# Performance work log

Measured on AMD Instinct MI355X. Metric: run time of the kernel, lower is better.

## Reference

```python
import jax, jax.numpy as jnp
import numpy as np

H_IN, W_IN = 128, 128  # sensor grid; region=(1,1), stride=(1,1) -> one RF per pixel


def setup_inputs() -> dict:
    key = jax.random.key(0)
    k1, k2, k3, k4, k5, k6 = jax.random.split(key, 6)
    B, N, C, HID = 8, 2048, 16, 128
    s = 1.0 / np.sqrt(HID)
    features = jax.random.normal(k1, (B, N, C), dtype=jnp.float32)
    coords = jax.random.randint(k2, (B, N, 2), 0, 128, dtype=jnp.int32)  # (x, y)
    w_ih = jax.random.normal(k3, (4 * HID, C), dtype=jnp.float32) * s
    w_hh = jax.random.normal(k4, (4 * HID, HID), dtype=jnp.float32) * s
    b_ih = jax.random.normal(k5, (4 * HID,), dtype=jnp.float32) * s
    b_hh = jax.random.normal(k6, (4 * HID,), dtype=jnp.float32) * s
    return {"features": features, "coords": coords, "w_ih": w_ih,
            "w_hh": w_hh, "b_ih": b_ih, "b_hh": b_hh}


def reference(features, coords, w_ih, w_hh, b_ih, b_hh):
    """MatrixLSTM with 1x1 non-overlapping receptive fields.

    Events (time-ordered along axis 1) are routed to their pixel's RF; a shared
    LSTM is run over each RF's event sequence and the last output per RF is
    scattered into a dense [B, hidden, H, W] map (zeros where no events).
    Implemented as one lax.scan over events with per-RF (h, c) state.
    """
    B, N, C = features.shape
    HID = w_hh.shape[1]
    # coord2idx: raster order y * W + x  -> RF id per event, [B, N]
    rf = coords[:, :, 1].astype(jnp.int32) * W_IN + coords[:, :, 0].astype(jnp.int32)
    bidx = jnp.arange(B)
    bias = b_ih + b_hh

    def step(carry, inp):
        h_all, c_all = carry              # [B, num_rf, HID] each
        x_t, rf_t = inp                   # [B, C], [B]
        h_prev = h_all[bidx, rf_t]        # gather per-RF state, [B, HID]
        c_prev = c_all[bidx, rf_t]
        gates = x_t @ w_ih.T + h_prev @ w_hh.T + bias  # [B, 4*HID]
        i, f, g, o = jnp.split(gates, 4, axis=-1)       # torch LSTM gate order
        i = jax.nn.sigmoid(i)
        f = jax.nn.sigmoid(f)
        g = jnp.tanh(g)
        o = jax.nn.sigmoid(o)
        c_new = f * c_prev + i * g
        h_new = o * jnp.tanh(c_new)
        h_all = h_all.at[bidx, rf_t].set(h_new)        # scatter back
        c_all = c_all.at[bidx, rf_t].set(c_new)
        return (h_all, c_all), None

    h0 = jnp.zeros((B, H_IN * W_IN, HID), features.dtype)
    c0 = jnp.zeros_like(h0)
    (h_all, _), _ = jax.lax.scan(step, (h0, c0),
                                 (features.transpose(1, 0, 2), rf.T))
    # final h per RF == LSTM output at each RF's last event; zeros if no events
    return h_all.reshape(B, H_IN, W_IN, HID).transpose(0, 3, 1, 2)
```

## Files before the change

kernel.cpp:

```cpp
#include <hip/hip_runtime.h>
#include <hip/hip_bf16.h>
#include <math.h>

#define B 8
#define N 2048
#define C 16
#define HID 128
#define NRF 16384
#define MAXLEN 8
#define MAXCH 2048

__global__ void k_init(int* __restrict__ cntrf, int* __restrict__ map,
                       int* __restrict__ cnt) {
    int i = blockIdx.x * blockDim.x + threadIdx.x;
    if (i < B * NRF) { cntrf[i] = 0; map[i] = -1; }
    if (i < B) cnt[i] = 0;
}

__global__ void k_prep(const float* __restrict__ w_ih, const float* __restrict__ w_hh,
                       const float* __restrict__ b_ih, const float* __restrict__ b_hh,
                       float* __restrict__ w_ih_T, float* __restrict__ w_hh_T,
                       float* __restrict__ biassum) {
    int idx = blockIdx.x * blockDim.x + threadIdx.x;
    if (idx < C * 512) {
        int c = idx >> 9, j = idx & 511;
        w_ih_T[idx] = w_ih[j * C + c];
    } else if (idx < C * 512 + HID * 512) {
        int t = idx - C * 512;
        int k = t >> 9, j = t & 511;
        w_hh_T[t] = w_hh[j * HID + k];
    } else if (idx < C * 512 + HID * 512 + 512) {
        int j = idx - (C * 512 + HID * 512);
        biassum[j] = b_ih[j] + b_hh[j];
    }
}

__global__ __launch_bounds__(256) void k_build(
    const int* __restrict__ coords, int* __restrict__ cntrf,
    int* __restrict__ map, int* __restrict__ cnt,
    int* __restrict__ chainrf, int* __restrict__ slots) {
    int idx = blockIdx.x * blockDim.x + threadIdx.x;
    int b = idx >> 11;
    int n = idx & (N - 1);
    int x = coords[idx * 2 + 0];
    int y = coords[idx * 2 + 1];
    int rf = y * 128 + x;
    int pos = atomicAdd(&cntrf[b * NRF + rf], 1);
    if (pos < MAXLEN) slots[(b * NRF + rf) * MAXLEN + pos] = n;

    __shared__ int lcnt, lbase;
    if (threadIdx.x == 0) lcnt = 0;
    __syncthreads();
    int r = -1;
    if (pos == 0) r = atomicAdd(&lcnt, 1);
    __syncthreads();
    if (threadIdx.x == 0) lbase = atomicAdd(&cnt[b], lcnt);
    __syncthreads();
    if (pos == 0) {
        int k = lbase + r;
        chainrf[b * MAXCH + k] = rf;
        map[b * NRF + rf] = k;
    }
}

__global__ __launch_bounds__(256) void k_gates(
    const float* __restrict__ features, const float* __restrict__ w_ih_T,
    const float* __restrict__ biassum, float* __restrict__ gates_x) {
    __shared__ float ls_w[C * 512];
    __shared__ float ls_b[512];
    __shared__ float ls_x[64 * C];
    int tid = threadIdx.x;
    for (int i = tid; i < C * 512; i += 256) ls_w[i] = w_ih_T[i];
    if (tid < 256) { ls_b[tid] = biassum[tid]; ls_b[tid + 256] = biassum[tid + 256]; }
    int e0 = blockIdx.x * 64;
    for (int i = tid; i < 64 * C; i += 256) ls_x[i] = features[e0 * C + i];
    __syncthreads();
    float b0 = ls_b[tid], b1 = ls_b[tid + 256];
    for (int e = 0; e < 64; e++) {
        float a0 = b0, a1 = b1;
#pragma unroll
        for (int ci = 0; ci < C; ci++) {
            float xv = ls_x[e * C + ci];
            a0 += ls_w[ci * 512 + tid] * xv;
            a1 += ls_w[ci * 512 + tid + 256] * xv;
        }
        gates_x[(size_t)(e0 + e) * 512 + tid] = a0;
        gates_x[(size_t)(e0 + e) * 512 + tid + 256] = a1;
    }
}

__global__ __launch_bounds__(64) void k_lstm(
    const float* __restrict__ gates_x, const float* __restrict__ w_hh_T,
    const int* __restrict__ cnt, const int* __restrict__ chainrf,
    const int* __restrict__ cntrf, const int* __restrict__ slots,
    float* __restrict__ hfin) {
    int b = blockIdx.x >> 9;
    int j0 = blockIdx.x & 511;
    int lane = threadIdx.x;
    __shared__ float lds_h[HID];
    int nch = cnt[b];
    for (int j = j0; j < nch; j += 512) {
        int rf = chainrf[b * MAXCH + j];
        int len = cntrf[b * NRF + rf];
        if (len > MAXLEN) len = MAXLEN;
        const int* sl = slots + (size_t)(b * NRF + rf) * MAXLEN;
        int ev[MAXLEN];
#pragma unroll
        for (int t = 0; t < MAXLEN; t++) {
            int v = sl[t];
            ev[t] = (t < len) ? v : 0x7fffffff;
        }
#pragma unroll
        for (int a = 0; a < MAXLEN; a++)
#pragma unroll
            for (int q = 0; q < MAXLEN - 1; q++) {
                int u = ev[q], v = ev[q + 1];
                ev[q] = min(u, v);
                ev[q + 1] = max(u, v);
            }
        float c0 = 0.f, c1 = 0.f, h0 = 0.f, h1 = 0.f;
#pragma unroll
        for (int t = 0; t < MAXLEN; t++) {
            if (t >= len) break;
            int n = ev[t];
            const float* gx = gates_x + (size_t)(b * N + n) * 512;
            float acc[8];
#pragma unroll
            for (int r = 0; r < 8; r++) acc[r] = gx[lane + 64 * r];
            if (t > 0) {
                for (int k = 0; k < HID; k += 2) {
                    float hv0 = lds_h[k];
                    float hv1 = lds_h[k + 1];
#pragma unroll
                    for (int r = 0; r < 8; r++)
                        acc[r] += w_hh_T[k * 512 + lane + 64 * r] * hv0;
#pragma unroll
                    for (int r = 0; r < 8; r++)
                        acc[r] += w_hh_T[(k + 1) * 512 + lane + 64 * r] * hv1;
                }
            }
            float i0 = 1.f / (1.f + expf(-acc[0]));
            float i1 = 1.f / (1.f + expf(-acc[1]));
            float f0 = 1.f / (1.f + expf(-acc[2]));
            float f1 = 1.f / (1.f + expf(-acc[3]));
            float g0 = tanhf(acc[4]);
            float g1 = tanhf(acc[5]);
            float o0 = 1.f / (1.f + expf(-acc[6]));
            float o1 = 1.f / (1.f + expf(-acc[7]));
            c0 = f0 * c0 + i0 * g0;
            c1 = f1 * c1 + i1 * g1;
            h0 = o0 * tanhf(c0);
            h1 = o1 * tanhf(c1);
            if (t + 1 < len) {
                __syncthreads();
                lds_h[lane] = h0;
                lds_h[lane + 64] = h1;
                __syncthreads();
            }
        }
        hfin[(size_t)(b * MAXCH + j) * HID + lane] = h0;
        hfin[(size_t)(b * MAXCH + j) * HID + lane + 64] = h1;
    }
}

__global__ __launch_bounds__(256) void k_scatter(
    const float* __restrict__ hfin, const int* __restrict__ map,
    float* __restrict__ out) {
    int b = blockIdx.x >> 7;
    int y = blockIdx.x & 127;
    int t = threadIdx.x;
    int xq = t & 31;
    int hg = t >> 5;
    const int4* mrow = (const int4*)(map + b * NRF + y * 128);
    int4 kk = mrow[xq];
    const float* hb = hfin + (size_t)b * MAXCH * HID;
#pragma unroll
    for (int hh = 0; hh < 16; hh++) {
        int hid = hg * 16 + hh;
        float4 v;
        v.x = (kk.x < 0) ? 0.f : hb[kk.x * HID + hid];
        v.y = (kk.y < 0) ? 0.f : hb[kk.y * HID + hid];
        v.z = (kk.z < 0) ? 0.f : hb[kk.z * HID + hid];
        v.w = (kk.w < 0) ? 0.f : hb[kk.w * HID + hid];
        *(float4*)(out + ((((size_t)b * HID + hid) * 128 + y) * 128) + xq * 4) = v;
    }
}

extern "C" void kernel_launch(void* const* d_in, const int* in_sizes, int n_in,
                              void* d_out, int out_size, void* d_ws, size_t ws_size,
                              hipStream_t stream) {
    const float* features = (const float*)d_in[0];
    const int*   coords   = (const int*)d_in[1];
    const float* w_ih     = (const float*)d_in[2];
    const float* w_hh     = (const float*)d_in[3];
    const float* b_ih     = (const float*)d_in[4];
    const float* b_hh     = (const float*)d_in[5];
    float* out = (float*)d_out;

    char* ws = (char*)d_ws;
    float* w_ih_T  = (float*)(ws + 0);
    float* w_hh_T  = (float*)(ws + 32768);
    float* biassum = (float*)(ws + 294912);
    int*   cntrf   = (int*)(ws + 296960);
    int*   map     = (int*)(ws + 821248);
    int*   cnt     = (int*)(ws + 1345536);
    int*   chainrf = (int*)(ws + 1345600);
    int*   slots   = (int*)(ws + 1411136);
    float* hfin    = (float*)(ws + 5605440);
    float* gates_x = (float*)(ws + 13994048);

    k_init<<<dim3((B * NRF + 255) / 256), dim3(256), 0, stream>>>(cntrf, map, cnt);
    k_prep<<<dim3((C * 512 + HID * 512 + 512 + 255) / 256), dim3(256), 0, stream>>>(
        w_ih, w_hh, b_ih, b_hh, w_ih_T, w_hh_T, biassum);
    k_build<<<dim3(B * N / 256), dim3(256), 0, stream>>>(
        coords, cntrf, map, cnt, chainrf, slots);
    k_gates<<<dim3(B * N / 64), dim3(256), 0, stream>>>(
        features, w_ih_T, biassum, gates_x);
    k_lstm<<<dim3(B * 512), dim3(64), 0, stream>>>(
        gates_x, w_hh_T, cnt, chainrf, cntrf, slots, hfin);
    k_scatter<<<dim3(B * 128), dim3(256), 0, stream>>>(hfin, map, out);
}
```

Baseline: 158.0 us.

## Split LSTM into single-event fast path and compacted multi-event kernel

```diff
diff --git a/kernel.cpp b/kernel.cpp
--- a/kernel.cpp
+++ b/kernel.cpp
@@ -10,72 +10,67 @@
 #define MAXLEN 8
 #define MAXCH 2048
 
-__global__ void k_init(int* __restrict__ cntrf, int* __restrict__ map,
-                       int* __restrict__ cnt) {
+__global__ __launch_bounds__(256) void k_setup(
+    const float* __restrict__ w_ih, const float* __restrict__ w_hh,
+    const float* __restrict__ b_ih, const float* __restrict__ b_hh,
+    float* __restrict__ w_ih_T, float* __restrict__ w_hh_T,
+    float* __restrict__ biassum, int* __restrict__ cntrf,
+    int* __restrict__ map, int* __restrict__ cnt, int* __restrict__ mcnt) {
     int i = blockIdx.x * blockDim.x + threadIdx.x;
-    if (i < B * NRF) { cntrf[i] = 0; map[i] = -1; }
+    cntrf[i] = 0;
+    map[i] = -1;
     if (i < B) cnt[i] = 0;
-}
-
-__global__ void k_prep(const float* __restrict__ w_ih, const float* __restrict__ w_hh,
-                       const float* __restrict__ b_ih, const float* __restrict__ b_hh,
-                       float* __restrict__ w_ih_T, float* __restrict__ w_hh_T,
-                       float* __restrict__ biassum) {
-    int idx = blockIdx.x * blockDim.x + threadIdx.x;
-    if (idx < C * 512) {
-        int c = idx >> 9, j = idx & 511;
-        w_ih_T[idx] = w_ih[j * C + c];
-    } else if (idx < C * 512 + HID * 512) {
-        int t = idx - C * 512;
-        int k = t >> 9, j = t & 511;
-        w_hh_T[t] = w_hh[j * HID + k];
-    } else if (idx < C * 512 + HID * 512 + 512) {
-        int j = idx - (C * 512 + HID * 512);
-        biassum[j] = b_ih[j] + b_hh[j];
-    }
-}
-
-__global__ __launch_bounds__(256) void k_build(
-    const int* __restrict__ coords, int* __restrict__ cntrf,
-    int* __restrict__ map, int* __restrict__ cnt,
-    int* __restrict__ chainrf, int* __restrict__ slots) {
-    int idx = blockIdx.x * blockDim.x + threadIdx.x;
-    int b = idx >> 11;
-    int n = idx & (N - 1);
-    int x = coords[idx * 2 + 0];
-    int y = coords[idx * 2 + 1];
-    int rf = y * 128 + x;
-    int pos = atomicAdd(&cntrf[b * NRF + rf], 1);
-    if (pos < MAXLEN) slots[(b * NRF + rf) * MAXLEN + pos] = n;
-
+    if (i == 0) mcnt[0] = 0;
+    if (i < C * 512) {
+        int c = i >> 9, j = i & 511;
+        w_ih_T[i] = w_ih[j * C + c];
+    }
+    if (i < HID * 512) {
+        int k = i >> 9, j = i & 511;
+        w_hh_T[i] = w_hh[j * HID + k];
+    }
+    if (i < 512) biassum[i] = b_ih[i] + b_hh[i];
+}
+
+__global__ __launch_bounds__(256) void k_buildgates(
+    const int* __restrict__ coords, const float* __restrict__ features,
+    const float* __restrict__ w_ih_T, const float* __restrict__ biassum,
+    int* __restrict__ cntrf, int* __restrict__ map, int* __restrict__ cnt,
+    int* __restrict__ chainrf, int* __restrict__ slots,
+    float* __restrict__ gates_x) {
+    int tid = threadIdx.x;
     __shared__ int lcnt, lbase;
-    if (threadIdx.x == 0) lcnt = 0;
-    __syncthreads();
-    int r = -1;
-    if (pos == 0) r = atomicAdd(&lcnt, 1);
-    __syncthreads();
-    if (threadIdx.x == 0) lbase = atomicAdd(&cnt[b], lcnt);
-    __syncthreads();
-    if (pos == 0) {
-        int k = lbase + r;
-        chainrf[b * MAXCH + k] = rf;
-        map[b * NRF + rf] = k;
-    }
-}
-
-__global__ __launch_bounds__(256) void k_gates(
-    const float* __restrict__ features, const float* __restrict__ w_ih_T,
-    const float* __restrict__ biassum, float* __restrict__ gates_x) {
     __shared__ float ls_w[C * 512];
-    __shared__ float ls_b[512];
     __shared__ float ls_x[64 * C];
-    int tid = threadIdx.x;
+
+    if (blockIdx.x < 64) {
+        int idx = blockIdx.x * 256 + tid;
+        int b = idx >> 11;
+        int n = idx & (N - 1);
+        int x = coords[idx * 2 + 0];
+        int y = coords[idx * 2 + 1];
+        int rf = y * 128 + x;
+        int pos = atomicAdd(&cntrf[b * NRF + rf], 1);
+        if (pos < MAXLEN) slots[(b * NRF + rf) * MAXLEN + pos] = n;
+        if (tid == 0) lcnt = 0;
+        __syncthreads();
+        int r = -1;
+        if (pos == 0) r = atomicAdd(&lcnt, 1);
+        __syncthreads();
+        if (tid == 0) lbase = atomicAdd(&cnt[b], lcnt);
+        __syncthreads();
+        if (pos == 0) {
+            int k = lbase + r;
+            chainrf[b * MAXCH + k] = rf;
+            map[b * NRF + rf] = k;
+        }
+    }
+
     for (int i = tid; i < C * 512; i += 256) ls_w[i] = w_ih_T[i];
-    if (tid < 256) { ls_b[tid] = biassum[tid]; ls_b[tid + 256] = biassum[tid + 256]; }
     int e0 = blockIdx.x * 64;
     for (int i = tid; i < 64 * C; i += 256) ls_x[i] = features[e0 * C + i];
-    __syncthreads();
-    float b0 = ls_b[tid], b1 = ls_b[tid + 256];
+    float b0 = biassum[tid], b1 = biassum[tid + 256];
+    __syncthreads();
     for (int e = 0; e < 64; e++) {
         float a0 = b0, a1 = b1;
 #pragma unroll
@@ -89,21 +84,79 @@
     }
 }
 
-__global__ __launch_bounds__(64) void k_lstm(
+__global__ __launch_bounds__(256) void k_classify(
+    const int* __restrict__ cnt, const int* __restrict__ chainrf,
+    const int* __restrict__ cntrf, int* __restrict__ mcnt,
+    int* __restrict__ mlist_brf, int* __restrict__ mlist_dst) {
+    int tid = threadIdx.x;
+    int idx = blockIdx.x * 256 + tid;
+    int b = idx >> 11, j = idx & (MAXCH - 1);
+    __shared__ int lcnt, lbase;
+    __shared__ int lbrf[256], ldst[256];
+    int len = 0, rf = 0;
+    if (j < cnt[b]) {
+        rf = chainrf[idx];
+        len = cntrf[b * NRF + rf];
+    }
+    if (tid == 0) lcnt = 0;
+    __syncthreads();
+    if (len >= 2) {
+        int r = atomicAdd(&lcnt, 1);
+        lbrf[r] = b * NRF + rf;
+        ldst[r] = idx;
+    }
+    __syncthreads();
+    if (tid == 0) lbase = atomicAdd(mcnt, lcnt);
+    __syncthreads();
+    for (int i = tid; i < lcnt; i += 256) {
+        mlist_brf[lbase + i] = lbrf[i];
+        mlist_dst[lbase + i] = ldst[i];
+    }
+}
+
+__global__ __launch_bounds__(256) void k_single(
+    const float* __restrict__ gates_x, const int* __restrict__ cnt,
+    const int* __restrict__ chainrf, const int* __restrict__ cntrf,
+    const int* __restrict__ slots, float* __restrict__ hfin) {
+    int lane = threadIdx.x & 63;
+    int wid = blockIdx.x * 4 + (threadIdx.x >> 6);
+    for (int ci = wid; ci < B * MAXCH; ci += 8192) {
+        int b = ci >> 11, j = ci & (MAXCH - 1);
+        if (j >= cnt[b]) continue;
+        int rf = chainrf[ci];
+        if (cntrf[b * NRF + rf] != 1) continue;
+        int n = slots[(size_t)(b * NRF + rf) * MAXLEN];
+        const float* gx = gates_x + (size_t)(b * N + n) * 512;
+        float i0 = gx[lane],       i1 = gx[lane + 64];
+        float g0 = gx[lane + 256], g1 = gx[lane + 320];
+        float o0 = gx[lane + 384], o1 = gx[lane + 448];
+        i0 = 1.f / (1.f + expf(-i0));
+        i1 = 1.f / (1.f + expf(-i1));
+        float c0 = i0 * tanhf(g0);
+        float c1 = i1 * tanhf(g1);
+        float h0 = (1.f / (1.f + expf(-o0))) * tanhf(c0);
+        float h1 = (1.f / (1.f + expf(-o1))) * tanhf(c1);
+        hfin[(size_t)ci * HID + lane] = h0;
+        hfin[(size_t)ci * HID + lane + 64] = h1;
+    }
+}
+
+__global__ __launch_bounds__(256) void k_multi(
     const float* __restrict__ gates_x, const float* __restrict__ w_hh_T,
-    const int* __restrict__ cnt, const int* __restrict__ chainrf,
-    const int* __restrict__ cntrf, const int* __restrict__ slots,
-    float* __restrict__ hfin) {
-    int b = blockIdx.x >> 9;
-    int j0 = blockIdx.x & 511;
-    int lane = threadIdx.x;
-    __shared__ float lds_h[HID];
-    int nch = cnt[b];
-    for (int j = j0; j < nch; j += 512) {
-        int rf = chainrf[b * MAXCH + j];
-        int len = cntrf[b * NRF + rf];
+    const int* __restrict__ mcnt, const int* __restrict__ mlist_brf,
+    const int* __restrict__ mlist_dst, const int* __restrict__ cntrf,
+    const int* __restrict__ slots, float* __restrict__ hfin) {
+    __shared__ float g512[512];
+    __shared__ float hbuf[HID];
+    int tid = threadIdx.x;
+    int M = mcnt[0];
+    for (int m = blockIdx.x; m < M; m += gridDim.x) {
+        int brf = mlist_brf[m];
+        int dst = mlist_dst[m];
+        int b = brf >> 14;
+        int len = cntrf[brf];
         if (len > MAXLEN) len = MAXLEN;
-        const int* sl = slots + (size_t)(b * NRF + rf) * MAXLEN;
+        const int* sl = slots + (size_t)brf * MAXLEN;
         int ev[MAXLEN];
 #pragma unroll
         for (int t = 0; t < MAXLEN; t++) {
@@ -118,48 +171,32 @@
                 ev[q] = min(u, v);
                 ev[q + 1] = max(u, v);
             }
-        float c0 = 0.f, c1 = 0.f, h0 = 0.f, h1 = 0.f;
-#pragma unroll
-        for (int t = 0; t < MAXLEN; t++) {
-            if (t >= len) break;
-            int n = ev[t];
-            const float* gx = gates_x + (size_t)(b * N + n) * 512;
-            float acc[8];
-#pragma unroll
-            for (int r = 0; r < 8; r++) acc[r] = gx[lane + 64 * r];
+        float c = 0.f;
+        for (int t = 0; t < len; t++) {
+            const float* gx = gates_x + (size_t)(b * N + ev[t]) * 512;
+            float a0 = gx[tid], a1 = gx[tid + 256];
             if (t > 0) {
-                for (int k = 0; k < HID; k += 2) {
-                    float hv0 = lds_h[k];
-                    float hv1 = lds_h[k + 1];
-#pragma unroll
-                    for (int r = 0; r < 8; r++)
-                        acc[r] += w_hh_T[k * 512 + lane + 64 * r] * hv0;
-#pragma unroll
-                    for (int r = 0; r < 8; r++)
-                        acc[r] += w_hh_T[(k + 1) * 512 + lane + 64 * r] * hv1;
+#pragma unroll 8
+                for (int k = 0; k < HID; k++) {
+                    float hv = hbuf[k];
+                    a0 += w_hh_T[k * 512 + tid] * hv;
+                    a1 += w_hh_T[k * 512 + tid + 256] * hv;
                 }
             }
-            float i0 = 1.f / (1.f + expf(-acc[0]));
-            float i1 = 1.f / (1.f + expf(-acc[1]));
-            float f0 = 1.f / (1.f + expf(-acc[2]));
-            float f1 = 1.f / (1.f + expf(-acc[3]));
-            float g0 = tanhf(acc[4]);
-            float g1 = tanhf(acc[5]);
-            float o0 = 1.f / (1.f + expf(-acc[6]));
-            float o1 = 1.f / (1.f + expf(-acc[7]));
-            c0 = f0 * c0 + i0 * g0;
-            c1 = f1 * c1 + i1 * g1;
-            h0 = o0 * tanhf(c0);
-            h1 = o1 * tanhf(c1);
-            if (t + 1 < len) {
-                __syncthreads();
-                lds_h[lane] = h0;
-                lds_h[lane + 64] = h1;
-                __syncthreads();
+            g512[tid] = a0;
+            g512[tid + 256] = a1;
+            __syncthreads();
+            if (tid < HID) {
+                float ig = 1.f / (1.f + expf(-g512[tid]));
+                float fg = 1.f / (1.f + expf(-g512[tid + 128]));
+                float gg = tanhf(g512[tid + 256]);
+                float og = 1.f / (1.f + expf(-g512[tid + 384]));
+                c = fg * c + ig * gg;
+                hbuf[tid] = og * tanhf(c);
             }
-        }
-        hfin[(size_t)(b * MAXCH + j) * HID + lane] = h0;
-        hfin[(size_t)(b * MAXCH + j) * HID + lane + 64] = h1;
+            __syncthreads();
+        }
+        if (tid < HID) hfin[(size_t)dst * HID + tid] = hbuf[tid];
     }
 }
 
@@ -198,25 +235,29 @@
     float* out = (float*)d_out;
 
     char* ws = (char*)d_ws;
-    float* w_ih_T  = (float*)(ws + 0);
-    float* w_hh_T  = (float*)(ws + 32768);
-    float* biassum = (float*)(ws + 294912);
-    int*   cntrf   = (int*)(ws + 296960);
-    int*   map     = (int*)(ws + 821248);
-    int*   cnt     = (int*)(ws + 1345536);
-    int*   chainrf = (int*)(ws + 1345600);
-    int*   slots   = (int*)(ws + 1411136);
-    float* hfin    = (float*)(ws + 5605440);
-    float* gates_x = (float*)(ws + 13994048);
-
-    k_init<<<dim3((B * NRF + 255) / 256), dim3(256), 0, stream>>>(cntrf, map, cnt);
-    k_prep<<<dim3((C * 512 + HID * 512 + 512 + 255) / 256), dim3(256), 0, stream>>>(
-        w_ih, w_hh, b_ih, b_hh, w_ih_T, w_hh_T, biassum);
-    k_build<<<dim3(B * N / 256), dim3(256), 0, stream>>>(
-        coords, cntrf, map, cnt, chainrf, slots);
-    k_gates<<<dim3(B * N / 64), dim3(256), 0, stream>>>(
-        features, w_ih_T, biassum, gates_x);
-    k_lstm<<<dim3(B * 512), dim3(64), 0, stream>>>(
-        gates_x, w_hh_T, cnt, chainrf, cntrf, slots, hfin);
+    float* w_ih_T    = (float*)(ws + 0);
+    float* w_hh_T    = (float*)(ws + 32768);
+    float* biassum   = (float*)(ws + 294912);
+    int*   cntrf     = (int*)(ws + 296960);
+    int*   map       = (int*)(ws + 821248);
+    int*   cnt       = (int*)(ws + 1345536);
+    int*   chainrf   = (int*)(ws + 1345600);
+    int*   slots     = (int*)(ws + 1411136);
+    float* hfin      = (float*)(ws + 5605440);
+    float* gates_x   = (float*)(ws + 13994048);
+    int*   mcnt      = (int*)(ws + 47548480);
+    int*   mlist_brf = (int*)(ws + 47548544);
+    int*   mlist_dst = (int*)(ws + 47614080);
+
+    k_setup<<<dim3(B * NRF / 256), dim3(256), 0, stream>>>(
+        w_ih, w_hh, b_ih, b_hh, w_ih_T, w_hh_T, biassum, cntrf, map, cnt, mcnt);
+    k_buildgates<<<dim3(B * N / 64), dim3(256), 0, stream>>>(
+        coords, features, w_ih_T, biassum, cntrf, map, cnt, chainrf, slots, gates_x);
+    k_classify<<<dim3(B * MAXCH / 256), dim3(256), 0, stream>>>(
+        cnt, chainrf, cntrf, mcnt, mlist_brf, mlist_dst);
+    k_single<<<dim3(2048), dim3(256), 0, stream>>>(
+        gates_x, cnt, chainrf, cntrf, slots, hfin);
+    k_multi<<<dim3(1024), dim3(256), 0, stream>>>(
+        gates_x, w_hh_T, mcnt, mlist_brf, mlist_dst, cntrf, slots, hfin);
     k_scatter<<<dim3(B * 128), dim3(256), 0, stream>>>(hfin, map, out);
 }
```

Result: faster. 144.5 us (-8.5%).
